# Optimization experiments

Hardware: AMD Instinct MI355X
Metric: run time of the kernel (lower is better)

## Reference

```python
import jax, jax.numpy as jnp
import numpy as np

T0 = 16
EPS = 1.1920929e-07  # torch fp32 finfo eps used by F.rms_norm default

def rmsnorm(v):
    return v * jax.lax.rsqrt(jnp.mean(v * v, axis=-1, keepdims=True) + EPS)

def apply_rotary_emb(x, cos, sin):
    # x: (B, S, H, C); rotate-half style as in source
    d = x.shape[-1] // 2
    x1, x2 = x[..., :d], x[..., d:]
    return jnp.concatenate([x1 * cos + x2 * sin, -x1 * sin + x2 * cos], axis=-1)

def setup_inputs():
    key = jax.random.key(0)
    ks = jax.random.split(key, 8)
    B, T, C, H = 8, 8192, 128, 8
    S = (T0 // 4) * T0 + 1  # 64 selected tokens + 1 sink = 65
    x = jax.random.normal(ks[0], (B, T, C), jnp.float32)
    # RoPE tables over the sink-augmented attention sequence, head_dim/2 = 64
    inv = 1.0 / (10000.0 ** (jnp.arange(C // 2, dtype=jnp.float32) / (C // 2)))
    ang = jnp.arange(S, dtype=jnp.float32)[:, None] * inv[None, :]
    cos = jnp.cos(ang)[None, :, None, :]  # (1, 65, 1, 64)
    sin = jnp.sin(ang)[None, :, None, :]
    sink = 0.02 * jax.random.normal(ks[1], (1, H, C), jnp.float32)
    W_qkvg = 0.02 * jax.random.normal(ks[2], (4 * C * H, C), jnp.float32)
    patch_w = 0.02 * jax.random.normal(ks[3], (T0 * C,), jnp.float32)
    W_out = 0.02 * jax.random.normal(ks[4], (C, H * C), jnp.float32)
    tao = jnp.array([1.2, 1.2], jnp.float32)
    return {"x": x, "cos": cos, "sin": sin, "sink": sink, "W_qkvg": W_qkvg,
            "patch_w": patch_w, "W_out": W_out, "tao": tao}

def reference(x, cos, sin, sink, W_qkvg, patch_w, W_out, tao):
    B, T, C = x.shape
    H = sink.shape[1]
    Np = T // T0  # T chosen as multiple of T0, so pad P = 0
    # --- patch scoring + topk patch selection (patch_toks) ---
    xp = x.reshape(B, Np, T0 * C)
    score = jax.nn.softmax(rmsnorm(xp) @ patch_w, axis=-1)  # (B, Np)
    _, I = jax.lax.top_k(score, T0 // 4)                    # top 4 patches
    I = jnp.sort(I, axis=-1)                                # (B, 4)
    # --- qkvg projection over ALL tokens, then patch-flattened chunk ---
    qkvg = x @ W_qkvg.T                                     # (B, T, 4*C*H)
    qkvg_p = qkvg.reshape(B, Np, 4 * T0 * C * H)
    n = T0 * C * H
    q_p = qkvg_p[..., 0 * n:1 * n]
    k_p = qkvg_p[..., 1 * n:2 * n]
    v_p = qkvg_p[..., 2 * n:3 * n]
    g_p = qkvg_p[..., 3 * n:4 * n]
    def gather(p):  # (B, Np, n) -> (B, 4*T0, H, C) via selected patches
        return jnp.take_along_axis(p, I[:, :, None], axis=1).reshape(B, -1, H, C)
    q, k, v, g = gather(q_p), gather(k_p), gather(v_p), gather(g_p)
    # --- sink token prepend ---
    s = jnp.broadcast_to(sink[:, None], (B, 1, H, C))
    q = jnp.concatenate([s, q], axis=1)  # (B, 65, H, C)
    k = jnp.concatenate([s, k], axis=1)
    v = jnp.concatenate([s, v], axis=1)
    # --- RoPE + RMSNorm + learned temperatures ---
    q = rmsnorm(apply_rotary_emb(q, cos, sin)) * tao[0]
    k = rmsnorm(apply_rotary_emb(k, cos, sin)) * tao[1]
    # --- causal SDPA (scale 1/sqrt(C)), drop sink row ---
    S = q.shape[1]
    att = jnp.einsum('bshc,bthc->bhst', q, k) / jnp.sqrt(jnp.float32(C))
    causal = jnp.tril(jnp.ones((S, S), dtype=bool))
    att = jax.nn.softmax(jnp.where(causal, att, -jnp.inf), axis=-1)
    y = jnp.einsum('bhst,bthc->bshc', att, v)[:, 1:]  # (B, 64, H, C)
    # --- sigmoid gating + output projection ---
    y = y * jax.nn.sigmoid(g)
    return y.reshape(B, y.shape[1], H * C) @ W_out.T  # (B, 64, C)
```

## Files before the change

kernel.cpp:

```cpp
#include <hip/hip_runtime.h>
#include <hip/hip_bf16.h>

#define EPSR 1.1920929e-07f

#define OFF_SCORE 0LL
#define OFF_WQT   8192LL
#define OFF_WO4   532480LL
#define OFF_SEL   663552LL
#define OFF_YG    4757504LL

__device__ __forceinline__ bool is_bf16_in(const void* tao) {
    unsigned int w = *(const unsigned int*)tao;
    return (w >> 16) == (w & 0xffffu);
}

__device__ __forceinline__ float ldin(const void* p, long long i, bool bf) {
    if (bf) return __uint_as_float(((unsigned int)(((const unsigned short*)p)[i])) << 16);
    return ((const float*)p)[i];
}

__device__ __forceinline__ float4 ldin4(const void* p, long long i, bool bf) {
    if (bf) {
        ushort4 u = ((const ushort4*)p)[i >> 2];
        return make_float4(__uint_as_float((unsigned int)u.x << 16),
                           __uint_as_float((unsigned int)u.y << 16),
                           __uint_as_float((unsigned int)u.z << 16),
                           __uint_as_float((unsigned int)u.w << 16));
    }
    return ((const float4*)p)[i >> 2];
}

__global__ __launch_bounds__(256) void k_prep_score(const void* Wq, const void* Wo,
                                                    const void* x, const void* pw,
                                                    const void* tao, float* ws) {
    bool bf = is_bf16_in(tao);
    __shared__ float tile[16448];
    int tid = threadIdx.x;
    if (blockIdx.x < 1024) {
        int lane = tid & 63, wid = tid >> 6;
        int patch = blockIdx.x * 4 + wid;
        long long base = (long long)patch * 2048;
        float ss = 0.f, dt = 0.f;
        #pragma unroll
        for (int i = 0; i < 8; i++) {
            int e = i * 256 + lane * 4;
            float4 v = ldin4(x, base + e, bf);
            float4 w = ldin4(pw, e, bf);
            ss += v.x * v.x + v.y * v.y + v.z * v.z + v.w * v.w;
            dt += v.x * w.x + v.y * w.y + v.z * w.z + v.w * w.w;
        }
        #pragma unroll
        for (int o = 32; o; o >>= 1) { ss += __shfl_xor(ss, o); dt += __shfl_xor(dt, o); }
        if (lane == 0) ws[OFF_SCORE + patch] = dt * rsqrtf(ss * (1.f / 2048.f) + EPSR);
    } else if (blockIdx.x < 1088) {
        float* WqT = ws + OFF_WQT;
        int j0 = (blockIdx.x - 1024) * 64;
        #pragma unroll
        for (int rep = 0; rep < 8; rep++) {
            int jr = rep * 8 + (tid >> 5);
            int c4 = (tid & 31) * 4;
            float4 v = ldin4(Wq, ((long long)(j0 + jr)) * 128 + c4, bf);
            float* t = &tile[jr * 129 + c4];
            t[0] = v.x; t[1] = v.y; t[2] = v.z; t[3] = v.w;
        }
        __syncthreads();
        #pragma unroll
        for (int rep = 0; rep < 8; rep++) {
            int c = rep * 16 + (tid >> 4);
            int jq = (tid & 15) * 4;
            float4 v = make_float4(tile[jq * 129 + c], tile[(jq + 1) * 129 + c],
                                   tile[(jq + 2) * 129 + c], tile[(jq + 3) * 129 + c]);
            *(float4*)&WqT[c * 4096 + j0 + jq] = v;
        }
    } else {
        float* Wo4 = ws + OFF_WO4;
        int co0 = (blockIdx.x - 1088) * 16;
        #pragma unroll
        for (int rep = 0; rep < 16; rep++) {
            float4 v = ldin4(Wo, ((long long)(co0 + rep)) * 1024 + tid * 4, bf);
            *(float4*)&tile[rep * 1028 + tid * 4] = v;
        }
        __syncthreads();
        #pragma unroll
        for (int rep = 0; rep < 16; rep++) {
            int idx = rep * 256 + tid;
            int fg = idx >> 4, co = idx & 15;
            float4 v = *(const float4*)&tile[co * 1028 + fg * 4];
            *(float4*)&Wo4[(fg * 128 + co0 + co) * 4] = v;
        }
    }
}

__global__ __launch_bounds__(256) void k_qkvg(const void* x, const void* cosp, const void* sinp,
                                              const void* tao, float* ws) {
    bool bf = is_bf16_in(tao);
    int blk = blockIdx.x;
    int jc = blk & 15, bp = blk >> 4;
    int b = bp >> 2, p = bp & 3;
    __shared__ float4 xs4[512];
    __shared__ int tok0s;
    int tid = threadIdx.x;
    if (tid < 64) {
        const float4* sp = (const float4*)(ws + OFF_SCORE + b * 512);
        float4 a = sp[tid * 2], c = sp[tid * 2 + 1];
        float v[8];
        v[0] = a.x; v[1] = a.y; v[2] = a.z; v[3] = a.w;
        v[4] = c.x; v[5] = c.y; v[6] = c.z; v[7] = c.w;
        int win[4];
        #pragma unroll
        for (int k = 0; k < 4; k++) {
            float bm = v[0]; int bi = 0;
            #pragma unroll
            for (int i = 1; i < 8; i++) if (v[i] > bm) { bm = v[i]; bi = i; }
            int gi = tid * 8 + bi;
            #pragma unroll
            for (int o = 32; o; o >>= 1) {
                float om = __shfl_xor(bm, o); int oi = __shfl_xor(gi, o);
                if (om > bm || (om == bm && oi < gi)) { bm = om; gi = oi; }
            }
            win[k] = gi;
            if ((gi >> 3) == tid) v[gi & 7] = -INFINITY;
        }
        if (tid == 0) {
            int a0 = win[0], a1 = win[1], a2 = win[2], a3 = win[3], tmp;
            if (a0 > a1) { tmp = a0; a0 = a1; a1 = tmp; }
            if (a2 > a3) { tmp = a2; a2 = a3; a3 = tmp; }
            if (a0 > a2) { tmp = a0; a0 = a2; a2 = tmp; }
            if (a1 > a3) { tmp = a1; a1 = a3; a3 = tmp; }
            if (a1 > a2) { tmp = a1; a1 = a2; a2 = tmp; }
            int sorted[4] = {a0, a1, a2, a3};
            tok0s = sorted[p] * 16;
        }
    }
    __syncthreads();
    int tok0 = tok0s;
    long long xbase = ((long long)(b * 8192 + tok0)) * 128;
    for (int i = tid; i < 512; i += 256)
        xs4[i] = ldin4(x, xbase + i * 4, bf);
    __syncthreads();
    int tg = tid >> 6, jx = tid & 63;
    const float4* WqT4 = (const float4*)(ws + OFF_WQT);
    int wcol = jc * 64 + jx;
    float4 acc[4];
    #pragma unroll
    for (int t = 0; t < 4; t++) acc[t] = make_float4(0.f, 0.f, 0.f, 0.f);
    float4 nw0 = WqT4[0 * 1024 + wcol];
    float4 nw1 = WqT4[1 * 1024 + wcol];
    float4 nw2 = WqT4[2 * 1024 + wcol];
    float4 nw3 = WqT4[3 * 1024 + wcol];
    for (int c4 = 0; c4 < 32; c4++) {
        float4 w0 = nw0, w1 = nw1, w2 = nw2, w3 = nw3;
        if (c4 < 31) {
            nw0 = WqT4[(c4 * 4 + 4) * 1024 + wcol];
            nw1 = WqT4[(c4 * 4 + 5) * 1024 + wcol];
            nw2 = WqT4[(c4 * 4 + 6) * 1024 + wcol];
            nw3 = WqT4[(c4 * 4 + 7) * 1024 + wcol];
        }
        #pragma unroll
        for (int t = 0; t < 4; t++) {
            float4 xv = xs4[(tg * 4 + t) * 32 + c4];
            acc[t].x += xv.x * w0.x + xv.y * w1.x + xv.z * w2.x + xv.w * w3.x;
            acc[t].y += xv.x * w0.y + xv.y * w1.y + xv.z * w2.y + xv.w * w3.y;
            acc[t].z += xv.x * w0.z + xv.y * w1.z + xv.z * w2.z + xv.w * w3.z;
            acc[t].w += xv.x * w0.w + xv.y * w1.w + xv.z * w2.w + xv.w * w3.w;
        }
    }
    if (tg < 2) {
        float taov = (tg == 0) ? ldin(tao, 0, bf) : ldin(tao, 1, bf);
        bool hi = (jx & 16) != 0;
        int cc4 = (jx & 15) * 4;
        int soff = jc >> 2;
        #pragma unroll
        for (int t = 0; t < 4; t++) {
            int s = p * 16 + t * 4 + soff + 1;
            float4 cs = ldin4(cosp, (long long)s * 64 + cc4, bf);
            float4 sn = ldin4(sinp, (long long)s * 64 + cc4, bf);
            float4 own = acc[t], prt;
            prt.x = __shfl_xor(own.x, 16);
            prt.y = __shfl_xor(own.y, 16);
            prt.z = __shfl_xor(own.z, 16);
            prt.w = __shfl_xor(own.w, 16);
            float4 r;
            if (!hi) {
                r.x = own.x * cs.x + prt.x * sn.x;
                r.y = own.y * cs.y + prt.y * sn.y;
                r.z = own.z * cs.z + prt.z * sn.z;
                r.w = own.w * cs.w + prt.w * sn.w;
            } else {
                r.x = own.x * cs.x - prt.x * sn.x;
                r.y = own.y * cs.y - prt.y * sn.y;
                r.z = own.z * cs.z - prt.z * sn.z;
                r.w = own.w * cs.w - prt.w * sn.w;
            }
            float ss = r.x * r.x + r.y * r.y + r.z * r.z + r.w * r.w;
            #pragma unroll
            for (int ofs = 16; ofs; ofs >>= 1) ss += __shfl_xor(ss, ofs);
            float sc = rsqrtf(ss * (1.f / 128.f) + EPSR) * taov;
            acc[t].x = r.x * sc; acc[t].y = r.y * sc;
            acc[t].z = r.z * sc; acc[t].w = r.w * sc;
        }
    }
    float4* sel4 = (float4*)(ws + OFF_SEL);
    #pragma unroll
    for (int t = 0; t < 4; t++)
        sel4[(bp * 16 + tg * 4 + t) * 1024 + wcol] = acc[t];
}

__global__ __launch_bounds__(512, 4) void k_fused(const void* sink, const void* tao, float* ws) {
    bool bf = is_bf16_in(tao);
    const float* sel = ws + OFF_SEL;
    const float4* sel4 = (const float4*)sel;
    float* yg = ws + OFF_YG;
    int blk = blockIdx.x;
    int b = blk >> 6, h = (blk >> 3) & 7, o = blk & 7;
    int smax = o * 8 + 8;
    int tid = threadIdx.x, lane = tid & 63, wid = tid >> 6;
    __shared__ float qs[8 * 132];
    __shared__ float ks[65 * 132];
    __shared__ float att[8 * 68];
    __shared__ float sinkv[128];

    if (tid < 128) sinkv[tid] = ldin(sink, h * 128 + tid, bf);
    for (int idx = tid; idx < smax * 32; idx += 512) {
        int row = (idx >> 5) + 1, c4 = idx & 31;
        int r = row - 1, pp = r >> 4, sl = r & 15;
        long long kb4 = (((long long)(b * 4 + pp) * 16 + 4 + (sl >> 2)) * 1024) + (sl & 3) * 256 + h * 32 + c4;
        *(float4*)&ks[row * 132 + c4 * 4] = sel4[kb4];
    }
    if (tid < 256) {
        int lr = tid >> 5, c4 = tid & 31;
        int r = o * 8 + lr;
        int pp = r >> 4, sl = r & 15;
        long long qb4 = (((long long)(b * 4 + pp) * 16 + (sl >> 2)) * 1024) + (sl & 3) * 256 + h * 32 + c4;
        *(float4*)&qs[lr * 132 + c4 * 4] = sel4[qb4];
    }
    if (tid >= 256 && tid < 288) {
        int l = tid - 256;
        float4 v = ldin4(sink, h * 128 + l * 4, bf);
        float ss = v.x * v.x + v.y * v.y + v.z * v.z + v.w * v.w;
        #pragma unroll
        for (int ofs = 16; ofs; ofs >>= 1) ss += __shfl_xor(ss, ofs);
        float sc = rsqrtf(ss * (1.f / 128.f) + EPSR) * ldin(tao, 1, bf);
        float* d = &ks[l * 4];
        d[0] = v.x * sc; d[1] = v.y * sc; d[2] = v.z * sc; d[3] = v.w * sc;
    }
    __syncthreads();

    {
        int ntiles = 4 * (4 * o + 5);
        if (tid < ntiles) {
            int sT = tid & 3, tT = tid >> 2;
            int ls0 = sT * 2;
            int s0g = o * 8 + 1 + ls0;
            int t0 = tT * 2;
            if (t0 <= s0g + 1) {
                int t1 = (t0 + 1 > smax) ? smax : t0 + 1;
                const float* q0 = &qs[ls0 * 132];
                const float* q1 = &qs[(ls0 + 1) * 132];
                const float* k0 = &ks[t0 * 132];
                const float* k1 = &ks[t1 * 132];
                float a00 = 0.f, a01 = 0.f, a10 = 0.f, a11 = 0.f;
                #pragma unroll 4
                for (int c = 0; c < 128; c += 4) {
                    float4 qa = *(const float4*)(q0 + c);
                    float4 qb = *(const float4*)(q1 + c);
                    float4 ka = *(const float4*)(k0 + c);
                    float4 kb = *(const float4*)(k1 + c);
                    a00 += qa.x * ka.x + qa.y * ka.y + qa.z * ka.z + qa.w * ka.w;
                    a01 += qa.x * kb.x + qa.y * kb.y + qa.z * kb.z + qa.w * kb.w;
                    a10 += qb.x * ka.x + qb.y * ka.y + qb.z * ka.z + qb.w * ka.w;
                    a11 += qb.x * kb.x + qb.y * kb.y + qb.z * kb.z + qb.w * kb.w;
                }
                const float scale = 0.08838834764831845f;
                if (t0 <= s0g)     att[ls0 * 68 + t0] = a00 * scale;
                if (t0 + 1 <= s0g) att[ls0 * 68 + t0 + 1] = a01 * scale;
                att[(ls0 + 1) * 68 + t0] = a10 * scale;
                if (t0 + 1 <= s0g + 1) att[(ls0 + 1) * 68 + t0 + 1] = a11 * scale;
            }
        }
    }
    __syncthreads();

    {
        int ls = wid;
        int s = o * 8 + 1 + ls;
        float x1 = (lane <= s) ? __expf(att[ls * 68 + lane]) : 0.f;
        float x2 = (lane == 0 && s == 64) ? __expf(att[ls * 68 + 64]) : 0.f;
        float sum = x1 + x2;
        #pragma unroll
        for (int ofs = 32; ofs; ofs >>= 1) sum += __shfl_xor(sum, ofs);
        float inv = 1.f / sum;
        att[ls * 68 + lane] = x1 * inv;
        if (lane < 4) att[ls * 68 + 64 + lane] = (lane == 0) ? x2 * inv : 0.f;
    }
    __syncthreads();

    if (tid < 256) {
        int row = tid >> 5, c0 = (tid & 31) * 4;
        const float* ar = &att[row * 68];
        float4 acc = make_float4(0.f, 0.f, 0.f, 0.f);
        {
            float4 a = *(const float4*)ar;
            float4 v0 = *(const float4*)&sinkv[c0];
            acc.x += a.x * v0.x; acc.y += a.x * v0.y; acc.z += a.x * v0.z; acc.w += a.x * v0.w;
            #pragma unroll
            for (int j = 1; j < 4; j++) {
                int r = j - 1;
                long long vb = (((long long)(b * 4) * 16 + 8 + (r >> 2)) * 4096) + (r & 3) * 1024 + h * 128 + c0;
                float4 vt = *(const float4*)&sel[vb];
                float aj = (j == 1) ? a.y : (j == 2) ? a.z : a.w;
                acc.x += aj * vt.x; acc.y += aj * vt.y; acc.z += aj * vt.z; acc.w += aj * vt.w;
            }
        }
        for (int t4 = 4; t4 <= smax - 4; t4 += 4) {
            float4 a = *(const float4*)(ar + t4);
            #pragma unroll
            for (int j = 0; j < 4; j++) {
                int r = t4 + j - 1;
                int pp = r >> 4, sl = r & 15;
                long long vb = (((long long)(b * 4 + pp) * 16 + 8 + (sl >> 2)) * 4096) + (sl & 3) * 1024 + h * 128 + c0;
                float4 vt = *(const float4*)&sel[vb];
                float aj = (j == 0) ? a.x : (j == 1) ? a.y : (j == 2) ? a.z : a.w;
                acc.x += aj * vt.x; acc.y += aj * vt.y; acc.z += aj * vt.z; acc.w += aj * vt.w;
            }
        }
        {
            float a = ar[smax];
            int r = smax - 1;
            int pp = r >> 4, sl = r & 15;
            long long vb = (((long long)(b * 4 + pp) * 16 + 8 + (sl >> 2)) * 4096) + (sl & 3) * 1024 + h * 128 + c0;
            float4 vt = *(const float4*)&sel[vb];
            acc.x += a * vt.x; acc.y += a * vt.y; acc.z += a * vt.z; acc.w += a * vt.w;
        }
        int rg = o * 8 + row;
        int pp = rg >> 4, sl = rg & 15, tl = 12 + (sl >> 2);
        long long gb = (((long long)(b * 4 + pp) * 16 + tl) * 4096) + (sl & 3) * 1024 + h * 128 + c0;
        float4 g = *(const float4*)&sel[gb];
        acc.x /= (1.f + __expf(-g.x));
        acc.y /= (1.f + __expf(-g.y));
        acc.z /= (1.f + __expf(-g.z));
        acc.w /= (1.f + __expf(-g.w));
        long long yb = ((long long)(b * 64 + rg)) * 1024 + h * 128 + c0;
        *(float4*)&yg[yb] = acc;
    }
}

__global__ __launch_bounds__(256) void k_out(const void* tao, float* ws, void* out) {
    bool bf = is_bf16_in(tao);
    int blk = blockIdx.x;
    int b = blk >> 5, rq = (blk >> 1) & 15, ch = blk & 1;
    int r0 = rq * 4, cbase = ch * 64;
    __shared__ float4 ylds[4 * 257];
    __shared__ float part[4][4][64];
    int tid = threadIdx.x;
    const float4* yg4 = (const float4*)(ws + OFF_YG);
    for (int i = tid; i < 1024; i += 256) {
        int row = i >> 8, f4 = i & 255;
        ylds[row * 257 + f4] = yg4[(b * 64 + r0 + row) * 256 + f4];
    }
    __syncthreads();
    int co4 = tid & 15, row = (tid >> 4) & 3, fs = tid >> 6;
    const float4* Wo44 = (const float4*)(ws + OFF_WO4);
    const float4* yrow = &ylds[row * 257];
    float a0 = 0.f, a1 = 0.f, a2 = 0.f, a3 = 0.f;
    int g0 = fs * 64;
    #pragma unroll 2
    for (int g = g0; g < g0 + 64; g++) {
        float4 y = yrow[g];
        const float4* wp = &Wo44[g * 128 + cbase + co4 * 4];
        float4 w0 = wp[0], w1 = wp[1], w2 = wp[2], w3 = wp[3];
        a0 += y.x * w0.x + y.y * w0.y + y.z * w0.z + y.w * w0.w;
        a1 += y.x * w1.x + y.y * w1.y + y.z * w1.z + y.w * w1.w;
        a2 += y.x * w2.x + y.y * w2.y + y.z * w2.z + y.w * w2.w;
        a3 += y.x * w3.x + y.y * w3.y + y.z * w3.z + y.w * w3.w;
    }
    part[fs][row][co4 * 4 + 0] = a0;
    part[fs][row][co4 * 4 + 1] = a1;
    part[fs][row][co4 * 4 + 2] = a2;
    part[fs][row][co4 * 4 + 3] = a3;
    __syncthreads();
    int row2 = tid >> 6, co = tid & 63;
    float v = part[0][row2][co] + part[1][row2][co] + part[2][row2][co] + part[3][row2][co];
    long long oidx = ((long long)(b * 64 + r0 + row2)) * 128 + cbase + co;
    if (bf) ((__hip_bfloat16*)out)[oidx] = __float2bfloat16(v);
    else    ((float*)out)[oidx] = v;
}

extern "C" void kernel_launch(void* const* d_in, const int* in_sizes, int n_in,
                              void* d_out, int out_size, void* d_ws, size_t ws_size,
                              hipStream_t stream) {
    const void* x    = d_in[0];
    const void* cosp = d_in[1];
    const void* sinp = d_in[2];
    const void* sink = d_in[3];
    const void* Wq   = d_in[4];
    const void* pw   = d_in[5];
    const void* Wo   = d_in[6];
    const void* tao  = d_in[7];
    float* ws = (float*)d_ws;

    k_prep_score<<<dim3(1096), dim3(256), 0, stream>>>(Wq, Wo, x, pw, tao, ws);
    k_qkvg <<<dim3(512), dim3(256), 0, stream>>>(x, cosp, sinp, tao, ws);
    k_fused<<<dim3(512), dim3(512), 0, stream>>>(sink, tao, ws);
    k_out  <<<dim3(256), dim3(256), 0, stream>>>(tao, ws, d_out);
}
```

Before: 141.2 us.

## Fuse four pipeline kernels into one cooperative kernel with grid syncs

Replaces the four separate launches (score/weight-transpose prep, qkvg projection, attention, output projection) with a single cooperative kernel of 512 blocks x 512 threads that separates the stages with grid.sync(). This removes the gaps between kernel launches and the per-launch overhead. The top-k selection stays inside each block as before. The trade-off is that grid-wide barriers force one fixed block shape on every stage, and the code falls back to the old four-kernel path if the cooperative launch fails.

```diff
diff --git a/kernel.cpp b/kernel.cpp
--- a/kernel.cpp
+++ b/kernel.cpp
@@ -1,5 +1,8 @@
 #include <hip/hip_runtime.h>
 #include <hip/hip_bf16.h>
+#include <hip/hip_cooperative_groups.h>
+
+namespace cg = cooperative_groups;
 
 #define EPSR 1.1920929e-07f
 
@@ -28,6 +31,380 @@
                            __uint_as_float((unsigned int)u.w << 16));
     }
     return ((const float4*)p)[i >> 2];
+}
+
+__global__ __launch_bounds__(512, 4) void k_all(const void* x, const void* cosp, const void* sinp,
+                                                const void* sink, const void* Wq, const void* pw,
+                                                const void* Wo, const void* tao, float* ws, void* out) {
+    cg::grid_group grid = cg::this_grid();
+    bool bf = is_bf16_in(tao);
+    __shared__ __align__(16) float lds[16448];
+    __shared__ int tok0s;
+    int tid = threadIdx.x;
+    int blk = blockIdx.x;
+
+    {
+        int lane = tid & 63, wid = tid >> 6;
+        int patch = blk * 8 + wid;
+        long long base = (long long)patch * 2048;
+        float ss = 0.f, dt = 0.f;
+        #pragma unroll
+        for (int i = 0; i < 8; i++) {
+            int e = i * 256 + lane * 4;
+            float4 v = ldin4(x, base + e, bf);
+            float4 w = ldin4(pw, e, bf);
+            ss += v.x * v.x + v.y * v.y + v.z * v.z + v.w * v.w;
+            dt += v.x * w.x + v.y * w.y + v.z * w.z + v.w * w.w;
+        }
+        #pragma unroll
+        for (int o = 32; o; o >>= 1) { ss += __shfl_xor(ss, o); dt += __shfl_xor(dt, o); }
+        if (lane == 0) ws[OFF_SCORE + patch] = dt * rsqrtf(ss * (1.f / 2048.f) + EPSR);
+    }
+    if (blk < 64) {
+        float* WqT = ws + OFF_WQT;
+        int j0 = blk * 64;
+        #pragma unroll
+        for (int rep = 0; rep < 4; rep++) {
+            int jr = rep * 16 + (tid >> 5);
+            int c4 = (tid & 31) * 4;
+            float4 v = ldin4(Wq, ((long long)(j0 + jr)) * 128 + c4, bf);
+            float* t = &lds[jr * 129 + c4];
+            t[0] = v.x; t[1] = v.y; t[2] = v.z; t[3] = v.w;
+        }
+        __syncthreads();
+        #pragma unroll
+        for (int rep = 0; rep < 4; rep++) {
+            int c = rep * 32 + (tid >> 4);
+            int jq = (tid & 15) * 4;
+            float4 v = make_float4(lds[jq * 129 + c], lds[(jq + 1) * 129 + c],
+                                   lds[(jq + 2) * 129 + c], lds[(jq + 3) * 129 + c]);
+            *(float4*)&WqT[c * 4096 + j0 + jq] = v;
+        }
+    } else if (blk < 72) {
+        float* Wo4 = ws + OFF_WO4;
+        int co0 = (blk - 64) * 16;
+        #pragma unroll
+        for (int rep = 0; rep < 8; rep++) {
+            int co = rep * 2 + (tid >> 8);
+            int f4 = (tid & 255) * 4;
+            float4 v = ldin4(Wo, ((long long)(co0 + co)) * 1024 + f4, bf);
+            *(float4*)&lds[co * 1028 + f4] = v;
+        }
+        __syncthreads();
+        #pragma unroll
+        for (int rep = 0; rep < 8; rep++) {
+            int idx = rep * 512 + tid;
+            int fg = idx >> 4, co = idx & 15;
+            float4 v = *(const float4*)&lds[co * 1028 + fg * 4];
+            *(float4*)&Wo4[(fg * 128 + co0 + co) * 4] = v;
+        }
+    }
+    grid.sync();
+
+    {
+        int jc = blk & 15, bp = blk >> 4;
+        int b = bp >> 2, p = bp & 3;
+        if (tid < 64) {
+            const float4* sp = (const float4*)(ws + OFF_SCORE + b * 512);
+            float4 a = sp[tid * 2], c = sp[tid * 2 + 1];
+            float v[8];
+            v[0] = a.x; v[1] = a.y; v[2] = a.z; v[3] = a.w;
+            v[4] = c.x; v[5] = c.y; v[6] = c.z; v[7] = c.w;
+            int win[4];
+            #pragma unroll
+            for (int k = 0; k < 4; k++) {
+                float bm = v[0]; int bi = 0;
+                #pragma unroll
+                for (int i = 1; i < 8; i++) if (v[i] > bm) { bm = v[i]; bi = i; }
+                int gi = tid * 8 + bi;
+                #pragma unroll
+                for (int o = 32; o; o >>= 1) {
+                    float om = __shfl_xor(bm, o); int oi = __shfl_xor(gi, o);
+                    if (om > bm || (om == bm && oi < gi)) { bm = om; gi = oi; }
+                }
+                win[k] = gi;
+                if ((gi >> 3) == tid) v[gi & 7] = -INFINITY;
+            }
+            if (tid == 0) {
+                int a0 = win[0], a1 = win[1], a2 = win[2], a3 = win[3], tmp;
+                if (a0 > a1) { tmp = a0; a0 = a1; a1 = tmp; }
+                if (a2 > a3) { tmp = a2; a2 = a3; a3 = tmp; }
+                if (a0 > a2) { tmp = a0; a0 = a2; a2 = tmp; }
+                if (a1 > a3) { tmp = a1; a1 = a3; a3 = tmp; }
+                if (a1 > a2) { tmp = a1; a1 = a2; a2 = tmp; }
+                int sorted[4] = {a0, a1, a2, a3};
+                tok0s = sorted[p] * 16;
+            }
+        }
+        __syncthreads();
+        int tok0 = tok0s;
+        long long xbase = ((long long)(b * 8192 + tok0)) * 128;
+        float4* xs4 = (float4*)lds;
+        xs4[tid] = ldin4(x, xbase + tid * 4, bf);
+        __syncthreads();
+        int tid8 = tid & 255, ch = tid >> 8;
+        int tg = tid8 >> 6, jx = tid8 & 63;
+        const float4* WqT4 = (const float4*)(ws + OFF_WQT);
+        int wcol = jc * 64 + jx;
+        float4 acc[4];
+        #pragma unroll
+        for (int t = 0; t < 4; t++) acc[t] = make_float4(0.f, 0.f, 0.f, 0.f);
+        int c0 = ch * 16;
+        float4 nw0 = WqT4[(c0 * 4 + 0) * 1024 + wcol];
+        float4 nw1 = WqT4[(c0 * 4 + 1) * 1024 + wcol];
+        float4 nw2 = WqT4[(c0 * 4 + 2) * 1024 + wcol];
+        float4 nw3 = WqT4[(c0 * 4 + 3) * 1024 + wcol];
+        for (int c4 = c0; c4 < c0 + 16; c4++) {
+            float4 w0 = nw0, w1 = nw1, w2 = nw2, w3 = nw3;
+            if (c4 < c0 + 15) {
+                nw0 = WqT4[(c4 * 4 + 4) * 1024 + wcol];
+                nw1 = WqT4[(c4 * 4 + 5) * 1024 + wcol];
+                nw2 = WqT4[(c4 * 4 + 6) * 1024 + wcol];
+                nw3 = WqT4[(c4 * 4 + 7) * 1024 + wcol];
+            }
+            #pragma unroll
+            for (int t = 0; t < 4; t++) {
+                float4 xv = xs4[(tg * 4 + t) * 32 + c4];
+                acc[t].x += xv.x * w0.x + xv.y * w1.x + xv.z * w2.x + xv.w * w3.x;
+                acc[t].y += xv.x * w0.y + xv.y * w1.y + xv.z * w2.y + xv.w * w3.y;
+                acc[t].z += xv.x * w0.z + xv.y * w1.z + xv.z * w2.z + xv.w * w3.z;
+                acc[t].w += xv.x * w0.w + xv.y * w1.w + xv.z * w2.w + xv.w * w3.w;
+            }
+        }
+        float4* red = (float4*)(lds + 2048);
+        if (ch == 1) {
+            #pragma unroll
+            for (int t = 0; t < 4; t++) red[tid8 * 4 + t] = acc[t];
+        }
+        __syncthreads();
+        if (ch == 0) {
+            #pragma unroll
+            for (int t = 0; t < 4; t++) {
+                float4 r = red[tid * 4 + t];
+                acc[t].x += r.x; acc[t].y += r.y; acc[t].z += r.z; acc[t].w += r.w;
+            }
+            if (tg < 2) {
+                float taov = (tg == 0) ? ldin(tao, 0, bf) : ldin(tao, 1, bf);
+                bool hi = (jx & 16) != 0;
+                int cc4 = (jx & 15) * 4;
+                int soff = jc >> 2;
+                #pragma unroll
+                for (int t = 0; t < 4; t++) {
+                    int s = p * 16 + t * 4 + soff + 1;
+                    float4 cs = ldin4(cosp, (long long)s * 64 + cc4, bf);
+                    float4 sn = ldin4(sinp, (long long)s * 64 + cc4, bf);
+                    float4 own = acc[t], prt;
+                    prt.x = __shfl_xor(own.x, 16);
+                    prt.y = __shfl_xor(own.y, 16);
+                    prt.z = __shfl_xor(own.z, 16);
+                    prt.w = __shfl_xor(own.w, 16);
+                    float4 r;
+                    if (!hi) {
+                        r.x = own.x * cs.x + prt.x * sn.x;
+                        r.y = own.y * cs.y + prt.y * sn.y;
+                        r.z = own.z * cs.z + prt.z * sn.z;
+                        r.w = own.w * cs.w + prt.w * sn.w;
+                    } else {
+                        r.x = own.x * cs.x - prt.x * sn.x;
+                        r.y = own.y * cs.y - prt.y * sn.y;
+                        r.z = own.z * cs.z - prt.z * sn.z;
+                        r.w = own.w * cs.w - prt.w * sn.w;
+                    }
+                    float ss = r.x * r.x + r.y * r.y + r.z * r.z + r.w * r.w;
+                    #pragma unroll
+                    for (int ofs = 16; ofs; ofs >>= 1) ss += __shfl_xor(ss, ofs);
+                    float sc = rsqrtf(ss * (1.f / 128.f) + EPSR) * taov;
+                    acc[t].x = r.x * sc; acc[t].y = r.y * sc;
+                    acc[t].z = r.z * sc; acc[t].w = r.w * sc;
+                }
+            }
+            float4* sel4w = (float4*)(ws + OFF_SEL);
+            #pragma unroll
+            for (int t = 0; t < 4; t++)
+                sel4w[(bp * 16 + tg * 4 + t) * 1024 + wcol] = acc[t];
+        }
+    }
+    grid.sync();
+
+    {
+        const float* sel = ws + OFF_SEL;
+        const float4* sel4 = (const float4*)sel;
+        float* yg = ws + OFF_YG;
+        int b = blk >> 6, h = (blk >> 3) & 7, o = blk & 7;
+        int smax = o * 8 + 8;
+        int lane = tid & 63, wid = tid >> 6;
+        float* qs = lds;
+        float* ks = lds + 1056;
+        float* att = lds + 9636;
+        float* sinkv = lds + 10180;
+
+        if (tid < 128) sinkv[tid] = ldin(sink, h * 128 + tid, bf);
+        for (int idx = tid; idx < smax * 32; idx += 512) {
+            int row = (idx >> 5) + 1, c4 = idx & 31;
+            int r = row - 1, pp = r >> 4, sl = r & 15;
+            long long kb4 = (((long long)(b * 4 + pp) * 16 + 4 + (sl >> 2)) * 1024) + (sl & 3) * 256 + h * 32 + c4;
+            *(float4*)&ks[row * 132 + c4 * 4] = sel4[kb4];
+        }
+        if (tid < 256) {
+            int lr = tid >> 5, c4 = tid & 31;
+            int r = o * 8 + lr;
+            int pp = r >> 4, sl = r & 15;
+            long long qb4 = (((long long)(b * 4 + pp) * 16 + (sl >> 2)) * 1024) + (sl & 3) * 256 + h * 32 + c4;
+            *(float4*)&qs[lr * 132 + c4 * 4] = sel4[qb4];
+        }
+        if (tid >= 256 && tid < 288) {
+            int l = tid - 256;
+            float4 v = ldin4(sink, h * 128 + l * 4, bf);
+            float ss = v.x * v.x + v.y * v.y + v.z * v.z + v.w * v.w;
+            #pragma unroll
+            for (int ofs = 16; ofs; ofs >>= 1) ss += __shfl_xor(ss, ofs);
+            float sc = rsqrtf(ss * (1.f / 128.f) + EPSR) * ldin(tao, 1, bf);
+            float* d = &ks[l * 4];
+            d[0] = v.x * sc; d[1] = v.y * sc; d[2] = v.z * sc; d[3] = v.w * sc;
+        }
+        __syncthreads();
+
+        {
+            int ntiles = 4 * (4 * o + 5);
+            if (tid < ntiles) {
+                int sT = tid & 3, tT = tid >> 2;
+                int ls0 = sT * 2;
+                int s0g = o * 8 + 1 + ls0;
+                int t0 = tT * 2;
+                if (t0 <= s0g + 1) {
+                    int t1 = (t0 + 1 > smax) ? smax : t0 + 1;
+                    const float* q0 = &qs[ls0 * 132];
+                    const float* q1 = &qs[(ls0 + 1) * 132];
+                    const float* k0 = &ks[t0 * 132];
+                    const float* k1 = &ks[t1 * 132];
+                    float a00 = 0.f, a01 = 0.f, a10 = 0.f, a11 = 0.f;
+                    #pragma unroll 4
+                    for (int c = 0; c < 128; c += 4) {
+                        float4 qa = *(const float4*)(q0 + c);
+                        float4 qb = *(const float4*)(q1 + c);
+                        float4 ka = *(const float4*)(k0 + c);
+                        float4 kb = *(const float4*)(k1 + c);
+                        a00 += qa.x * ka.x + qa.y * ka.y + qa.z * ka.z + qa.w * ka.w;
+                        a01 += qa.x * kb.x + qa.y * kb.y + qa.z * kb.z + qa.w * kb.w;
+                        a10 += qb.x * ka.x + qb.y * ka.y + qb.z * ka.z + qb.w * ka.w;
+                        a11 += qb.x * kb.x + qb.y * kb.y + qb.z * kb.z + qb.w * kb.w;
+                    }
+                    const float scale = 0.08838834764831845f;
+                    if (t0 <= s0g)     att[ls0 * 68 + t0] = a00 * scale;
+                    if (t0 + 1 <= s0g) att[ls0 * 68 + t0 + 1] = a01 * scale;
+                    att[(ls0 + 1) * 68 + t0] = a10 * scale;
+                    if (t0 + 1 <= s0g + 1) att[(ls0 + 1) * 68 + t0 + 1] = a11 * scale;
+                }
+            }
+        }
+        __syncthreads();
+
+        {
+            int ls = wid;
+            int s = o * 8 + 1 + ls;
+            float x1 = (lane <= s) ? __expf(att[ls * 68 + lane]) : 0.f;
+            float x2 = (lane == 0 && s == 64) ? __expf(att[ls * 68 + 64]) : 0.f;
+            float sum = x1 + x2;
+            #pragma unroll
+            for (int ofs = 32; ofs; ofs >>= 1) sum += __shfl_xor(sum, ofs);
+            float inv = 1.f / sum;
+            att[ls * 68 + lane] = x1 * inv;
+            if (lane < 4) att[ls * 68 + 64 + lane] = (lane == 0) ? x2 * inv : 0.f;
+        }
+        __syncthreads();
+
+        if (tid < 256) {
+            int row = tid >> 5, c0 = (tid & 31) * 4;
+            const float* ar = &att[row * 68];
+            float4 acc = make_float4(0.f, 0.f, 0.f, 0.f);
+            {
+                float4 a = *(const float4*)ar;
+                float4 v0 = *(const float4*)&sinkv[c0];
+                acc.x += a.x * v0.x; acc.y += a.x * v0.y; acc.z += a.x * v0.z; acc.w += a.x * v0.w;
+                #pragma unroll
+                for (int j = 1; j < 4; j++) {
+                    int r = j - 1;
+                    long long vb = (((long long)(b * 4) * 16 + 8 + (r >> 2)) * 4096) + (r & 3) * 1024 + h * 128 + c0;
+                    float4 vt = *(const float4*)&sel[vb];
+                    float aj = (j == 1) ? a.y : (j == 2) ? a.z : a.w;
+                    acc.x += aj * vt.x; acc.y += aj * vt.y; acc.z += aj * vt.z; acc.w += aj * vt.w;
+                }
+            }
+            for (int t4 = 4; t4 <= smax - 4; t4 += 4) {
+                float4 a = *(const float4*)(ar + t4);
+                #pragma unroll
+                for (int j = 0; j < 4; j++) {
+                    int r = t4 + j - 1;
+                    int pp = r >> 4, sl = r & 15;
+                    long long vb = (((long long)(b * 4 + pp) * 16 + 8 + (sl >> 2)) * 4096) + (sl & 3) * 1024 + h * 128 + c0;
+                    float4 vt = *(const float4*)&sel[vb];
+                    float aj = (j == 0) ? a.x : (j == 1) ? a.y : (j == 2) ? a.z : a.w;
+                    acc.x += aj * vt.x; acc.y += aj * vt.y; acc.z += aj * vt.z; acc.w += aj * vt.w;
+                }
+            }
+            {
+                float a = ar[smax];
+                int r = smax - 1;
+                int pp = r >> 4, sl = r & 15;
+                long long vb = (((long long)(b * 4 + pp) * 16 + 8 + (sl >> 2)) * 4096) + (sl & 3) * 1024 + h * 128 + c0;
+                float4 vt = *(const float4*)&sel[vb];
+                acc.x += a * vt.x; acc.y += a * vt.y; acc.z += a * vt.z; acc.w += a * vt.w;
+            }
+            int rg = o * 8 + row;
+            int pp = rg >> 4, sl = rg & 15, tl = 12 + (sl >> 2);
+            long long gb = (((long long)(b * 4 + pp) * 16 + tl) * 4096) + (sl & 3) * 1024 + h * 128 + c0;
+            float4 g = *(const float4*)&sel[gb];
+            acc.x /= (1.f + __expf(-g.x));
+            acc.y /= (1.f + __expf(-g.y));
+            acc.z /= (1.f + __expf(-g.z));
+            acc.w /= (1.f + __expf(-g.w));
+            long long yb = ((long long)(b * 64 + rg)) * 1024 + h * 128 + c0;
+            *(float4*)&yg[yb] = acc;
+        }
+    }
+    grid.sync();
+
+    if (blk < 256) {
+        int b = blk >> 5, rq = (blk >> 1) & 15, chh = blk & 1;
+        int r0 = rq * 4, cbase = chh * 64;
+        float4* ylds = (float4*)lds;
+        float* part = lds + 4112;
+        const float4* yg4 = (const float4*)(ws + OFF_YG);
+        for (int i = tid; i < 1024; i += 512) {
+            int row = i >> 8, f4 = i & 255;
+            ylds[row * 257 + f4] = yg4[(b * 64 + r0 + row) * 256 + f4];
+        }
+        __syncthreads();
+        int co4 = tid & 15, row = (tid >> 4) & 3, fs = tid >> 6;
+        const float4* Wo44 = (const float4*)(ws + OFF_WO4);
+        const float4* yrow = &ylds[row * 257];
+        float a0 = 0.f, a1 = 0.f, a2 = 0.f, a3 = 0.f;
+        int g0 = fs * 32;
+        #pragma unroll 2
+        for (int g = g0; g < g0 + 32; g++) {
+            float4 y = yrow[g];
+            const float4* wp = &Wo44[g * 128 + cbase + co4 * 4];
+            float4 w0 = wp[0], w1 = wp[1], w2 = wp[2], w3 = wp[3];
+            a0 += y.x * w0.x + y.y * w0.y + y.z * w0.z + y.w * w0.w;
+            a1 += y.x * w1.x + y.y * w1.y + y.z * w1.z + y.w * w1.w;
+            a2 += y.x * w2.x + y.y * w2.y + y.z * w2.z + y.w * w2.w;
+            a3 += y.x * w3.x + y.y * w3.y + y.z * w3.z + y.w * w3.w;
+        }
+        part[(fs * 4 + row) * 64 + co4 * 4 + 0] = a0;
+        part[(fs * 4 + row) * 64 + co4 * 4 + 1] = a1;
+        part[(fs * 4 + row) * 64 + co4 * 4 + 2] = a2;
+        part[(fs * 4 + row) * 64 + co4 * 4 + 3] = a3;
+        __syncthreads();
+        if (tid < 256) {
+            int row2 = tid >> 6, co = tid & 63;
+            float v = 0.f;
+            #pragma unroll
+            for (int f = 0; f < 8; f++) v += part[(f * 4 + row2) * 64 + co];
+            long long oidx = ((long long)(b * 64 + r0 + row2)) * 128 + cbase + co;
+            if (bf) ((__hip_bfloat16*)out)[oidx] = __float2bfloat16(v);
+            else    ((float*)out)[oidx] = v;
+        }
+    }
 }
 
 __global__ __launch_bounds__(256) void k_prep_score(const void* Wq, const void* Wo,
@@ -398,9 +775,17 @@
     const void* Wo   = d_in[6];
     const void* tao  = d_in[7];
     float* ws = (float*)d_ws;
-
-    k_prep_score<<<dim3(1096), dim3(256), 0, stream>>>(Wq, Wo, x, pw, tao, ws);
-    k_qkvg <<<dim3(512), dim3(256), 0, stream>>>(x, cosp, sinp, tao, ws);
-    k_fused<<<dim3(512), dim3(512), 0, stream>>>(sink, tao, ws);
-    k_out  <<<dim3(256), dim3(256), 0, stream>>>(tao, ws, d_out);
-}
+    void* outp = d_out;
+
+    void* kargs[] = {(void*)&x, (void*)&cosp, (void*)&sinp, (void*)&sink,
+                     (void*)&Wq, (void*)&pw, (void*)&Wo, (void*)&tao,
+                     (void*)&ws, (void*)&outp};
+    hipError_t err = hipLaunchCooperativeKernel((const void*)k_all, dim3(512), dim3(512),
+                                                kargs, 0, stream);
+    if (err != hipSuccess) {
+        k_prep_score<<<dim3(1096), dim3(256), 0, stream>>>(Wq, Wo, x, pw, tao, ws);
+        k_qkvg <<<dim3(512), dim3(256), 0, stream>>>(x, cosp, sinp, tao, ws);
+        k_fused<<<dim3(512), dim3(512), 0, stream>>>(sink, tao, ws);
+        k_out  <<<dim3(256), dim3(256), 0, stream>>>(tao, ws, d_out);
+    }
+}
```

Measured after the change: 355.0 us. +151.5%, slower.

## Balance causal attention work by pairing early and late query rows per block

Applied to the files above, without the earlier changes.

Each attention block now takes four query rows from the front of the sequence and four from the back (u and 15-u), so every block does the same causal work instead of a load that grows with the block index. The PV accumulation is split across both halves of the 512-thread block, with keys 0-31 and 32-64 handled separately and the partial sums combined through shared memory before gating. All 64 key rows are now loaded for every block, and the change adds an extra barrier and a small shared buffer.

```diff
diff --git a/kernel.cpp b/kernel.cpp
--- a/kernel.cpp
+++ b/kernel.cpp
@@ -212,16 +212,16 @@
     const float4* sel4 = (const float4*)sel;
     float* yg = ws + OFF_YG;
     int blk = blockIdx.x;
-    int b = blk >> 6, h = (blk >> 3) & 7, o = blk & 7;
-    int smax = o * 8 + 8;
+    int b = blk >> 6, h = (blk >> 3) & 7, u = blk & 7;
     int tid = threadIdx.x, lane = tid & 63, wid = tid >> 6;
     __shared__ float qs[8 * 132];
     __shared__ float ks[65 * 132];
     __shared__ float att[8 * 68];
     __shared__ float sinkv[128];
+    __shared__ float4 part[8][32];
 
     if (tid < 128) sinkv[tid] = ldin(sink, h * 128 + tid, bf);
-    for (int idx = tid; idx < smax * 32; idx += 512) {
+    for (int idx = tid; idx < 64 * 32; idx += 512) {
         int row = (idx >> 5) + 1, c4 = idx & 31;
         int r = row - 1, pp = r >> 4, sl = r & 15;
         long long kb4 = (((long long)(b * 4 + pp) * 16 + 4 + (sl >> 2)) * 1024) + (sl & 3) * 256 + h * 32 + c4;
@@ -229,7 +229,7 @@
     }
     if (tid < 256) {
         int lr = tid >> 5, c4 = tid & 31;
-        int r = o * 8 + lr;
+        int r = (lr < 4) ? (u * 4 + lr) : ((15 - u) * 4 + (lr - 4));
         int pp = r >> 4, sl = r & 15;
         long long qb4 = (((long long)(b * 4 + pp) * 16 + (sl >> 2)) * 1024) + (sl & 3) * 256 + h * 32 + c4;
         *(float4*)&qs[lr * 132 + c4 * 4] = sel4[qb4];
@@ -246,44 +246,41 @@
     }
     __syncthreads();
 
-    {
-        int ntiles = 4 * (4 * o + 5);
-        if (tid < ntiles) {
-            int sT = tid & 3, tT = tid >> 2;
-            int ls0 = sT * 2;
-            int s0g = o * 8 + 1 + ls0;
-            int t0 = tT * 2;
-            if (t0 <= s0g + 1) {
-                int t1 = (t0 + 1 > smax) ? smax : t0 + 1;
-                const float* q0 = &qs[ls0 * 132];
-                const float* q1 = &qs[(ls0 + 1) * 132];
-                const float* k0 = &ks[t0 * 132];
-                const float* k1 = &ks[t1 * 132];
-                float a00 = 0.f, a01 = 0.f, a10 = 0.f, a11 = 0.f;
-                #pragma unroll 4
-                for (int c = 0; c < 128; c += 4) {
-                    float4 qa = *(const float4*)(q0 + c);
-                    float4 qb = *(const float4*)(q1 + c);
-                    float4 ka = *(const float4*)(k0 + c);
-                    float4 kb = *(const float4*)(k1 + c);
-                    a00 += qa.x * ka.x + qa.y * ka.y + qa.z * ka.z + qa.w * ka.w;
-                    a01 += qa.x * kb.x + qa.y * kb.y + qa.z * kb.z + qa.w * kb.w;
-                    a10 += qb.x * ka.x + qb.y * ka.y + qb.z * ka.z + qb.w * ka.w;
-                    a11 += qb.x * kb.x + qb.y * kb.y + qb.z * kb.z + qb.w * kb.w;
-                }
-                const float scale = 0.08838834764831845f;
-                if (t0 <= s0g)     att[ls0 * 68 + t0] = a00 * scale;
-                if (t0 + 1 <= s0g) att[ls0 * 68 + t0 + 1] = a01 * scale;
-                att[(ls0 + 1) * 68 + t0] = a10 * scale;
-                if (t0 + 1 <= s0g + 1) att[(ls0 + 1) * 68 + t0 + 1] = a11 * scale;
-            }
+    if (tid < 132) {
+        int sT = tid & 3, tT = tid >> 2;
+        int lsp = sT * 2;
+        int s0g = (lsp < 4) ? (u * 4 + 1 + lsp) : ((15 - u) * 4 + 1 + (lsp - 4));
+        int t0 = tT * 2;
+        if (t0 <= s0g + 1) {
+            int t1 = (t0 + 1 > 64) ? 64 : t0 + 1;
+            const float* q0 = &qs[lsp * 132];
+            const float* q1 = &qs[(lsp + 1) * 132];
+            const float* k0 = &ks[t0 * 132];
+            const float* k1 = &ks[t1 * 132];
+            float a00 = 0.f, a01 = 0.f, a10 = 0.f, a11 = 0.f;
+            #pragma unroll 4
+            for (int c = 0; c < 128; c += 4) {
+                float4 qa = *(const float4*)(q0 + c);
+                float4 qb = *(const float4*)(q1 + c);
+                float4 ka = *(const float4*)(k0 + c);
+                float4 kb = *(const float4*)(k1 + c);
+                a00 += qa.x * ka.x + qa.y * ka.y + qa.z * ka.z + qa.w * ka.w;
+                a01 += qa.x * kb.x + qa.y * kb.y + qa.z * kb.z + qa.w * kb.w;
+                a10 += qb.x * ka.x + qb.y * ka.y + qb.z * ka.z + qb.w * ka.w;
+                a11 += qb.x * kb.x + qb.y * kb.y + qb.z * kb.z + qb.w * kb.w;
+            }
+            const float scale = 0.08838834764831845f;
+            if (t0 <= s0g)     att[lsp * 68 + t0] = a00 * scale;
+            if (t0 + 1 <= s0g) att[lsp * 68 + t0 + 1] = a01 * scale;
+            att[(lsp + 1) * 68 + t0] = a10 * scale;
+            if (t0 + 1 <= s0g + 1) att[(lsp + 1) * 68 + t0 + 1] = a11 * scale;
         }
     }
     __syncthreads();
 
     {
         int ls = wid;
-        int s = o * 8 + 1 + ls;
+        int s = (ls < 4) ? (u * 4 + 1 + ls) : ((15 - u) * 4 + 1 + (ls - 4));
         float x1 = (lane <= s) ? __expf(att[ls * 68 + lane]) : 0.f;
         float x2 = (lane == 0 && s == 64) ? __expf(att[ls * 68 + 64]) : 0.f;
         float sum = x1 + x2;
@@ -295,53 +292,78 @@
     }
     __syncthreads();
 
-    if (tid < 256) {
-        int row = tid >> 5, c0 = (tid & 31) * 4;
+    {
+        int th = tid >> 8;
+        int row = (tid >> 5) & 7, c0 = (tid & 31) * 4;
+        int s = (row < 4) ? (u * 4 + 1 + row) : ((15 - u) * 4 + 1 + (row - 4));
         const float* ar = &att[row * 68];
         float4 acc = make_float4(0.f, 0.f, 0.f, 0.f);
-        {
-            float4 a = *(const float4*)ar;
-            float4 v0 = *(const float4*)&sinkv[c0];
-            acc.x += a.x * v0.x; acc.y += a.x * v0.y; acc.z += a.x * v0.z; acc.w += a.x * v0.w;
+        if (th == 0) {
+            {
+                float4 a = *(const float4*)ar;
+                float4 v0 = *(const float4*)&sinkv[c0];
+                acc.x += a.x * v0.x; acc.y += a.x * v0.y; acc.z += a.x * v0.z; acc.w += a.x * v0.w;
+                #pragma unroll
+                for (int j = 1; j < 4; j++) {
+                    int r = j - 1;
+                    long long vb = (((long long)(b * 4) * 16 + 8 + (r >> 2)) * 4096) + (r & 3) * 1024 + h * 128 + c0;
+                    float4 vt = *(const float4*)&sel[vb];
+                    float aj = (j == 1) ? a.y : (j == 2) ? a.z : a.w;
+                    acc.x += aj * vt.x; acc.y += aj * vt.y; acc.z += aj * vt.z; acc.w += aj * vt.w;
+                }
+            }
             #pragma unroll
-            for (int j = 1; j < 4; j++) {
-                int r = j - 1;
-                long long vb = (((long long)(b * 4) * 16 + 8 + (r >> 2)) * 4096) + (r & 3) * 1024 + h * 128 + c0;
-                float4 vt = *(const float4*)&sel[vb];
-                float aj = (j == 1) ? a.y : (j == 2) ? a.z : a.w;
-                acc.x += aj * vt.x; acc.y += aj * vt.y; acc.z += aj * vt.z; acc.w += aj * vt.w;
-            }
-        }
-        for (int t4 = 4; t4 <= smax - 4; t4 += 4) {
-            float4 a = *(const float4*)(ar + t4);
+            for (int t4 = 4; t4 <= 28; t4 += 4) {
+                float4 a = *(const float4*)(ar + t4);
+                #pragma unroll
+                for (int j = 0; j < 4; j++) {
+                    int r = t4 + j - 1;
+                    int pp = r >> 4, sl = r & 15;
+                    long long vb = (((long long)(b * 4 + pp) * 16 + 8 + (sl >> 2)) * 4096) + (sl & 3) * 1024 + h * 128 + c0;
+                    float4 vt = *(const float4*)&sel[vb];
+                    float aj = (j == 0) ? a.x : (j == 1) ? a.y : (j == 2) ? a.z : a.w;
+                    acc.x += aj * vt.x; acc.y += aj * vt.y; acc.z += aj * vt.z; acc.w += aj * vt.w;
+                }
+            }
+        } else if (s >= 32) {
             #pragma unroll
-            for (int j = 0; j < 4; j++) {
-                int r = t4 + j - 1;
+            for (int t4 = 32; t4 <= 60; t4 += 4) {
+                float4 a = *(const float4*)(ar + t4);
+                #pragma unroll
+                for (int j = 0; j < 4; j++) {
+                    int r = t4 + j - 1;
+                    int pp = r >> 4, sl = r & 15;
+                    long long vb = (((long long)(b * 4 + pp) * 16 + 8 + (sl >> 2)) * 4096) + (sl & 3) * 1024 + h * 128 + c0;
+                    float4 vt = *(const float4*)&sel[vb];
+                    float aj = (j == 0) ? a.x : (j == 1) ? a.y : (j == 2) ? a.z : a.w;
+                    acc.x += aj * vt.x; acc.y += aj * vt.y; acc.z += aj * vt.z; acc.w += aj * vt.w;
+                }
+            }
+            {
+                float a = ar[64];
+                int r = 63;
                 int pp = r >> 4, sl = r & 15;
                 long long vb = (((long long)(b * 4 + pp) * 16 + 8 + (sl >> 2)) * 4096) + (sl & 3) * 1024 + h * 128 + c0;
                 float4 vt = *(const float4*)&sel[vb];
-                float aj = (j == 0) ? a.x : (j == 1) ? a.y : (j == 2) ? a.z : a.w;
-                acc.x += aj * vt.x; acc.y += aj * vt.y; acc.z += aj * vt.z; acc.w += aj * vt.w;
-            }
-        }
-        {
-            float a = ar[smax];
-            int r = smax - 1;
-            int pp = r >> 4, sl = r & 15;
-            long long vb = (((long long)(b * 4 + pp) * 16 + 8 + (sl >> 2)) * 4096) + (sl & 3) * 1024 + h * 128 + c0;
-            float4 vt = *(const float4*)&sel[vb];
-            acc.x += a * vt.x; acc.y += a * vt.y; acc.z += a * vt.z; acc.w += a * vt.w;
-        }
-        int rg = o * 8 + row;
-        int pp = rg >> 4, sl = rg & 15, tl = 12 + (sl >> 2);
-        long long gb = (((long long)(b * 4 + pp) * 16 + tl) * 4096) + (sl & 3) * 1024 + h * 128 + c0;
-        float4 g = *(const float4*)&sel[gb];
-        acc.x /= (1.f + __expf(-g.x));
-        acc.y /= (1.f + __expf(-g.y));
-        acc.z /= (1.f + __expf(-g.z));
-        acc.w /= (1.f + __expf(-g.w));
-        long long yb = ((long long)(b * 64 + rg)) * 1024 + h * 128 + c0;
-        *(float4*)&yg[yb] = acc;
+                acc.x += a * vt.x; acc.y += a * vt.y; acc.z += a * vt.z; acc.w += a * vt.w;
+            }
+        }
+        if (th == 1) part[row][tid & 31] = acc;
+        __syncthreads();
+        if (th == 0) {
+            float4 pr = part[row][tid & 31];
+            acc.x += pr.x; acc.y += pr.y; acc.z += pr.z; acc.w += pr.w;
+            int rg = s - 1;
+            int pp = rg >> 4, sl = rg & 15, tl = 12 + (sl >> 2);
+            long long gb = (((long long)(b * 4 + pp) * 16 + tl) * 4096) + (sl & 3) * 1024 + h * 128 + c0;
+            float4 g = *(const float4*)&sel[gb];
+            acc.x /= (1.f + __expf(-g.x));
+            acc.y /= (1.f + __expf(-g.y));
+            acc.z /= (1.f + __expf(-g.z));
+            acc.w /= (1.f + __expf(-g.w));
+            long long yb = ((long long)(b * 64 + rg)) * 1024 + h * 128 + c0;
+            *(float4*)&yg[yb] = acc;
+        }
     }
 }
 
```

After: 137.8 us. 2.4% less time.
